# Performance work log

Hardware: AMD Instinct MI355X
Metric: run time of the kernel (lower is better)

The kernel has to match this reference:

```python
import jax, jax.numpy as jnp
import numpy as np

N_NODES = 50000
N_EDGES = 800000
D_IN = 128
D_H = 128
D_OUT = 1
N_GRAPHS = 64
BN_EPS = 1e-5


def _lin(key, i, o):
    return jax.random.normal(key, (i, o), jnp.float32) / np.float32(np.sqrt(i))


def setup_inputs() -> dict:
    key = jax.random.key(0)
    ks = jax.random.split(key, 40)
    inp = {}
    inp["x"] = jax.random.normal(ks[0], (N_NODES, D_IN), jnp.float32)
    inp["edge_index"] = jax.random.randint(ks[1], (2, N_EDGES), 0, N_NODES)
    inp["batch"] = jnp.sort(jax.random.randint(ks[2], (N_NODES,), 0, N_GRAPHS))
    dims = [D_IN, D_H, D_H]
    ki = 3
    for l in range(3):
        inp[f"l{l}_W1"] = _lin(ks[ki], dims[l], D_H); ki += 1
        inp[f"l{l}_b1"] = jnp.zeros((D_H,), jnp.float32)
        inp[f"l{l}_W2"] = _lin(ks[ki], D_H, D_H); ki += 1
        inp[f"l{l}_b2"] = jnp.zeros((D_H,), jnp.float32)
        inp[f"l{l}_g"] = jnp.ones((D_H,), jnp.float32)
        inp[f"l{l}_beta"] = jnp.zeros((D_H,), jnp.float32)
    inp["p_W1"] = _lin(ks[ki], D_H * 3, D_H); ki += 1
    inp["p_b1"] = jnp.zeros((D_H,), jnp.float32)
    inp["p_g"] = jnp.ones((D_H,), jnp.float32)
    inp["p_beta"] = jnp.zeros((D_H,), jnp.float32)
    inp["p_W2"] = _lin(ks[ki], D_H, D_OUT); ki += 1
    inp["p_b2"] = jnp.zeros((D_OUT,), jnp.float32)
    return inp


def _bn(h, g, b):
    # training-mode BatchNorm1d: biased batch statistics over dim 0
    m = h.mean(0)
    v = h.var(0)
    return (h - m) * (g / jnp.sqrt(v + BN_EPS)) + b


def _gin_conv(x, src, dst, W1, b1, W2, b2):
    # scatter-add neighbor aggregation: messages x[src] summed into dst
    agg = jax.ops.segment_sum(x[src], dst, num_segments=N_NODES)
    h = x + agg  # eps = 0 (GINConv default)
    h = jax.nn.relu(h @ W1 + b1)
    return h @ W2 + b2


def reference(x, edge_index, batch,
              l0_W1, l0_b1, l0_W2, l0_b2, l0_g, l0_beta,
              l1_W1, l1_b1, l1_W2, l1_b2, l1_g, l1_beta,
              l2_W1, l2_b1, l2_W2, l2_b2, l2_g, l2_beta,
              p_W1, p_b1, p_g, p_beta, p_W2, p_b2):
    src, dst = edge_index[0], edge_index[1]
    layers = [
        (l0_W1, l0_b1, l0_W2, l0_b2, l0_g, l0_beta),
        (l1_W1, l1_b1, l1_W2, l1_b2, l1_g, l1_beta),
        (l2_W1, l2_b1, l2_W2, l2_b2, l2_g, l2_beta),
    ]
    h = x
    h_list = []
    for (W1, b1, W2, b2, g, beta) in layers:
        h = _gin_conv(h, src, dst, W1, b1, W2, b2)
        h = jax.nn.relu(_bn(h, g, beta))
        # dropout: identity in eval mode
        h_list.append(h)
    # global mean pool per layer, then concat
    cnt = jax.ops.segment_sum(jnp.ones((N_NODES,), jnp.float32), batch,
                              num_segments=N_GRAPHS)
    cnt = jnp.maximum(cnt, 1.0)[:, None]
    pooled = [jax.ops.segment_sum(hh, batch, num_segments=N_GRAPHS) / cnt
              for hh in h_list]
    z = jnp.concatenate(pooled, axis=1)  # [G, 3*D_H]
    # prediction MLP: fc1 -> relu -> bn -> fc2 (dropout identity)
    z = jax.nn.relu(z @ p_W1 + p_b1)
    z = _bn(z, p_g, p_beta)
    return z @ p_W2 + p_b2  # [G, D_OUT]
```

## Files before the change

kernel.cpp:

```cpp
#include <hip/hip_runtime.h>

#define NN 50000
#define NE 800000
#define D  128
#define NG 64
#define BN_EPS 1e-5f
#define SCAN_B 196

typedef __attribute__((ext_vector_type(8))) short short8;
typedef __attribute__((ext_vector_type(4))) float f32x4;

static __device__ inline unsigned short f2bf_rn(float f) {
  unsigned u = __float_as_uint(f);
  unsigned r = (u + 0x7FFF + ((u >> 16) & 1)) >> 16;
  return (unsigned short)r;
}
static __device__ inline float bf2f(unsigned short h) {
  return __uint_as_float((unsigned)h << 16);
}

__global__ void k_hist(const int* __restrict__ dst, int* __restrict__ counts) {
  int e = blockIdx.x * blockDim.x + threadIdx.x;
  if (e < NE) atomicAdd(&counts[dst[e]], 1);
}

__global__ void k_scan1(const int* __restrict__ counts, int* __restrict__ bsum) {
  const int t = threadIdx.x;
  const int i = blockIdx.x * 256 + t;
  int v = (i < NN) ? counts[i] : 0;
  #pragma unroll
  for (int d = 32; d >= 1; d >>= 1) v += __shfl_xor(v, d, 64);
  __shared__ int ws[4];
  if ((t & 63) == 0) ws[t >> 6] = v;
  __syncthreads();
  if (t == 0) bsum[blockIdx.x] = ws[0] + ws[1] + ws[2] + ws[3];
}

__global__ void k_scan2(const int* __restrict__ bsum, int* __restrict__ boff,
                        int* __restrict__ offs) {
  const int t = threadIdx.x, lane = t & 63, w = t >> 6;
  int v = (t < SCAN_B) ? bsum[t] : 0;
  int s = v;
  #pragma unroll
  for (int d = 1; d < 64; d <<= 1) { int u = __shfl_up(s, d, 64); if (lane >= d) s += u; }
  __shared__ int ws[4];
  if (lane == 63) ws[w] = s;
  __syncthreads();
  int add = 0;
  for (int k = 0; k < w; ++k) add += ws[k];
  if (t < SCAN_B) boff[t] = add + s - v;
  if (t == SCAN_B - 1) offs[NN] = add + s;
}

__global__ void k_scan3(const int* __restrict__ counts, const int* __restrict__ boff,
                        int* __restrict__ offs) {
  const int t = threadIdx.x, lane = t & 63, w = t >> 6;
  const int i = blockIdx.x * 256 + t;
  int v = (i < NN) ? counts[i] : 0;
  int s = v;
  #pragma unroll
  for (int d = 1; d < 64; d <<= 1) { int u = __shfl_up(s, d, 64); if (lane >= d) s += u; }
  __shared__ int ws[4];
  if (lane == 63) ws[w] = s;
  __syncthreads();
  int add = 0;
  for (int k = 0; k < w; ++k) add += ws[k];
  if (i < NN) offs[i] = boff[blockIdx.x] + add + s - v;
}

__global__ void k_scatter(const int* __restrict__ src, const int* __restrict__ dst,
                          const int* __restrict__ offs, int* __restrict__ cursor,
                          int* __restrict__ esrc) {
  int e = blockIdx.x * blockDim.x + threadIdx.x;
  if (e < NE) {
    int d = dst[e];
    int p = offs[d] + atomicAdd(&cursor[d], 1);
    esrc[p] = src[e];
  }
}

__global__ void k_gbounds(const int* __restrict__ batch, int* __restrict__ gstart) {
  const int g = threadIdx.x;
  if (g > NG) return;
  int lo = 0, hi = NN;
  while (lo < hi) { int mid = (lo + hi) >> 1; if (batch[mid] < g) lo = mid + 1; else hi = mid; }
  gstart[g] = lo;
}

__global__ __launch_bounds__(256) void k_cvt(const float* __restrict__ X,
                                             unsigned long long* __restrict__ Xb) {
  const int n4 = NN * D / 4;
  for (int i = blockIdx.x * blockDim.x + threadIdx.x; i < n4; i += gridDim.x * blockDim.x) {
    float4 v = ((const float4*)X)[i];
    unsigned long long p = (unsigned long long)f2bf_rn(v.x) |
                           ((unsigned long long)f2bf_rn(v.y) << 16) |
                           ((unsigned long long)f2bf_rn(v.z) << 32) |
                           ((unsigned long long)f2bf_rn(v.w) << 48);
    Xb[i] = p;
  }
}

struct WPtrs { const float* w[6]; };
__global__ void k_prep6(WPtrs ws, short* __restrict__ wb) {
  const int widx = blockIdx.y;
  const float* __restrict__ W = ws.w[widx];
  short* __restrict__ Wh = wb + (size_t)(widx * 2) * 16384;
  short* __restrict__ Wl = Wh + 16384;
  const int idx = blockIdx.x * 256 + threadIdx.x;
  const int k = idx >> 7, c = idx & 127;
  const float v = W[idx];
  const unsigned short h = f2bf_rn(v);
  const unsigned short lo = f2bf_rn(v - bf2f(h));
  const int o = ((k >> 5) * 128 + c) * 32 + (k & 31);
  Wh[o] = (short)h;
  Wl[o] = (short)lo;
}

template<bool BN>
__global__ __launch_bounds__(256) void k_aggregate(const unsigned* __restrict__ Hb,
                                                   const int* __restrict__ offs,
                                                   const int* __restrict__ esrc,
                                                   const float* __restrict__ sums,
                                                   const float* __restrict__ sumsq,
                                                   const float* __restrict__ gw,
                                                   const float* __restrict__ beta,
                                                   float* __restrict__ zstats,
                                                   unsigned* __restrict__ AGGh,
                                                   unsigned* __restrict__ AGGl) {
  if (blockIdx.x == 0 && threadIdx.x < 256) zstats[threadIdx.x] = 0.f;

  const int node = blockIdx.x * 4 + (threadIdx.x >> 6);
  const int lane = threadIdx.x & 63;
  float2 sc = make_float2(1.f, 1.f), sh = make_float2(0.f, 0.f);
  if (BN) {
    const float2 s2 = ((const float2*)sums)[lane];
    const float2 q2 = ((const float2*)sumsq)[lane];
    const float2 g2 = ((const float2*)gw)[lane];
    const float2 b2 = ((const float2*)beta)[lane];
    const float mx = s2.x * (1.f / NN), my = s2.y * (1.f / NN);
    sc.x = g2.x / sqrtf(q2.x * (1.f / NN) - mx * mx + BN_EPS);
    sc.y = g2.y / sqrtf(q2.y * (1.f / NN) - my * my + BN_EPS);
    sh.x = b2.x - mx * sc.x;
    sh.y = b2.y - my * sc.y;
  }

  auto rd = [&](int r) -> float2 {
    const unsigned u = Hb[r * 64 + lane];
    float2 v = make_float2(bf2f((unsigned short)u), bf2f((unsigned short)(u >> 16)));
    if (BN) {
      v.x = fmaxf(fmaf(v.x, sc.x, sh.x), 0.f);
      v.y = fmaxf(fmaf(v.y, sc.y, sh.y), 0.f);
    }
    return v;
  };

  float2 acc = rd(node);
  const int b = offs[node], e = offs[node + 1];
  int i = b;
  for (; i + 8 <= e; i += 8) {
    const int s0 = esrc[i],     s1 = esrc[i + 1], s2 = esrc[i + 2], s3 = esrc[i + 3];
    const int s4 = esrc[i + 4], s5 = esrc[i + 5], s6 = esrc[i + 6], s7 = esrc[i + 7];
    const float2 v0 = rd(s0), v1 = rd(s1), v2 = rd(s2), v3 = rd(s3);
    const float2 v4 = rd(s4), v5 = rd(s5), v6 = rd(s6), v7 = rd(s7);
    acc.x += ((v0.x + v1.x) + (v2.x + v3.x)) + ((v4.x + v5.x) + (v6.x + v7.x));
    acc.y += ((v0.y + v1.y) + (v2.y + v3.y)) + ((v4.y + v5.y) + (v6.y + v7.y));
  }
  for (; i + 4 <= e; i += 4) {
    const int s0 = esrc[i], s1 = esrc[i + 1], s2 = esrc[i + 2], s3 = esrc[i + 3];
    const float2 v0 = rd(s0), v1 = rd(s1), v2 = rd(s2), v3 = rd(s3);
    acc.x += (v0.x + v1.x) + (v2.x + v3.x);
    acc.y += (v0.y + v1.y) + (v2.y + v3.y);
  }
  for (; i < e; ++i) {
    const float2 v = rd(esrc[i]);
    acc.x += v.x; acc.y += v.y;
  }
  const unsigned short hx = f2bf_rn(acc.x), hy = f2bf_rn(acc.y);
  AGGh[node * 64 + lane] = (unsigned)hx | ((unsigned)hy << 16);
  const unsigned short lx = f2bf_rn(acc.x - bf2f(hx)), ly = f2bf_rn(acc.y - bf2f(hy));
  AGGl[node * 64 + lane] = (unsigned)lx | ((unsigned)ly << 16);
}

__global__ __launch_bounds__(512) void k_mlp2(const short* __restrict__ Ah,
                                              const short* __restrict__ Al,
                                              const short* __restrict__ W1h, const short* __restrict__ W1l,
                                              const short* __restrict__ W2h, const short* __restrict__ W2l,
                                              const float* __restrict__ b1, const float* __restrict__ b2,
                                              short* __restrict__ Hb,
                                              float* __restrict__ stats) {
  __shared__ __align__(16) short regA[32768];
  __shared__ __align__(16) short regB[32768];

  const int t = threadIdx.x;
  {
    const short8* __restrict__ g1h = (const short8*)W1h;
    const short8* __restrict__ g1l = (const short8*)W1l;
    const short8* __restrict__ g2h = (const short8*)W2h;
    const short8* __restrict__ g2l = (const short8*)W2l;
    short8* a8 = (short8*)regA;
    short8* b8 = (short8*)regB;
    #pragma unroll
    for (int i = 0; i < 4; ++i) {
      a8[i * 512 + t]        = g1h[i * 512 + t];
      a8[2048 + i * 512 + t] = g1l[i * 512 + t];
      b8[i * 512 + t]        = g2h[i * 512 + t];
      b8[2048 + i * 512 + t] = g2l[i * 512 + t];
    }
  }

  const int l = t & 63, w = t >> 6;
  const int lr = l & 15, fq = l >> 4, lk = fq * 8;
  const int tile0 = blockIdx.x * 128 + w * 16;
  const int arow = tile0 + lr;
  const bool rowok = arow < NN;

  short8 ah[4], al[4];
  {
    const short8 z = (short8)(0);
    #pragma unroll
    for (int kc = 0; kc < 4; ++kc) {
      ah[kc] = rowok ? *(const short8*)(Ah + (size_t)arow * D + kc * 32 + lk) : z;
      al[kc] = rowok ? *(const short8*)(Al + (size_t)arow * D + kc * 32 + lk) : z;
    }
  }
  __syncthreads();

  f32x4 acc[8];
  #pragma unroll
  for (int ct = 0; ct < 8; ++ct) acc[ct] = (f32x4)(0.f);
  #pragma unroll
  for (int kc = 0; kc < 4; ++kc) {
    #pragma unroll
    for (int ct = 0; ct < 8; ++ct) {
      const short8 bh = *(const short8*)(&regA[(kc * 128 + ct * 16 + lr) * 32 + lk]);
      const short8 bl = *(const short8*)(&regA[16384 + (kc * 128 + ct * 16 + lr) * 32 + lk]);
      acc[ct] = __builtin_amdgcn_mfma_f32_16x16x32_bf16(ah[kc], bh, acc[ct], 0, 0, 0);
      acc[ct] = __builtin_amdgcn_mfma_f32_16x16x32_bf16(al[kc], bh, acc[ct], 0, 0, 0);
      acc[ct] = __builtin_amdgcn_mfma_f32_16x16x32_bf16(ah[kc], bl, acc[ct], 0, 0, 0);
    }
  }
  __syncthreads();

  #pragma unroll
  for (int ct = 0; ct < 8; ++ct) {
    const float bb = b1[ct * 16 + lr];
    #pragma unroll
    for (int j = 0; j < 4; ++j) {
      const int r = w * 16 + fq * 4 + j;
      const int swc = (ct * 16 + lr) ^ ((r & 7) << 3);
      const float v = fmaxf(acc[ct][j] + bb, 0.f);
      const unsigned short h = f2bf_rn(v);
      regA[r * 128 + swc] = (short)h;
      regA[16384 + r * 128 + swc] = (short)f2bf_rn(v - bf2f(h));
    }
  }
  __syncthreads();

  f32x4 acc2[8];
  #pragma unroll
  for (int ct = 0; ct < 8; ++ct) acc2[ct] = (f32x4)(0.f);
  {
    const int r = w * 16 + lr;
    const int sx = (r & 7) << 3;
    short8 ch[4], cl[4];
    #pragma unroll
    for (int kc = 0; kc < 4; ++kc) {
      const int swb = r * 128 + ((kc * 32 + lk) ^ sx);
      ch[kc] = *(const short8*)(regA + swb);
      cl[kc] = *(const short8*)(regA + 16384 + swb);
    }
    #pragma unroll
    for (int kc = 0; kc < 4; ++kc) {
      #pragma unroll
      for (int ct = 0; ct < 8; ++ct) {
        const short8 bh = *(const short8*)(&regB[(kc * 128 + ct * 16 + lr) * 32 + lk]);
        const short8 bl = *(const short8*)(&regB[16384 + (kc * 128 + ct * 16 + lr) * 32 + lk]);
        acc2[ct] = __builtin_amdgcn_mfma_f32_16x16x32_bf16(ch[kc], bh, acc2[ct], 0, 0, 0);
        acc2[ct] = __builtin_amdgcn_mfma_f32_16x16x32_bf16(cl[kc], bh, acc2[ct], 0, 0, 0);
        acc2[ct] = __builtin_amdgcn_mfma_f32_16x16x32_bf16(ch[kc], bl, acc2[ct], 0, 0, 0);
      }
    }
  }

  float ps[8], pq[8];
  #pragma unroll
  for (int ct = 0; ct < 8; ++ct) { ps[ct] = 0.f; pq[ct] = 0.f; }
  #pragma unroll
  for (int ct = 0; ct < 8; ++ct) {
    const float bb = b2[ct * 16 + lr];
    #pragma unroll
    for (int j = 0; j < 4; ++j) {
      const int gr = tile0 + fq * 4 + j;
      if (gr < NN) {
        const float v = acc2[ct][j] + bb;
        Hb[(size_t)gr * D + ct * 16 + lr] = (short)f2bf_rn(v);
        ps[ct] += v; pq[ct] += v * v;
      }
    }
  }
  __syncthreads();
  float* red  = (float*)regA;
  float* redq = red + 4096;
  const int grp = w * 4 + fq;
  #pragma unroll
  for (int ct = 0; ct < 8; ++ct) {
    red [grp * 128 + ct * 16 + lr] = ps[ct];
    redq[grp * 128 + ct * 16 + lr] = pq[ct];
  }
  __syncthreads();
  if (t < 128) {
    float s = 0.f, q = 0.f;
    #pragma unroll
    for (int g2 = 0; g2 < 32; ++g2) { s += red[g2 * 128 + t]; q += redq[g2 * 128 + t]; }
    atomicAdd(&stats[t], s);
    atomicAdd(&stats[128 + t], q);
  }
}

__global__ __launch_bounds__(256) void k_pool(const unsigned short* __restrict__ Hb,
                                              const float* __restrict__ sums,
                                              const float* __restrict__ sumsq,
                                              const float* __restrict__ gw,
                                              const float* __restrict__ beta,
                                              const int* __restrict__ gstart,
                                              float* __restrict__ pooled, int lofs) {
  const int g = blockIdx.y;
  const int s = gstart[g], e = gstart[g + 1];
  const int t = threadIdx.x, c = t & 127, half = t >> 7;
  const float m  = sums[c] * (1.f / NN);
  const float sc = gw[c] / sqrtf(sumsq[c] * (1.f / NN) - m * m + BN_EPS);
  const float sh = beta[c] - m * sc;
  const int len = e - s;
  const int nchunk = (int)gridDim.x;
  const int per = (len + nchunk - 1) / nchunk;
  const int r0 = s + (int)blockIdx.x * per;
  const int r1 = min(e, r0 + per);
  float sum = 0.f;
  for (int r = r0 + half; r < r1; r += 2)
    sum += fmaxf(fmaf(bf2f(Hb[r * D + c]), sc, sh), 0.f);
  __shared__ float red[256];
  red[t] = sum;
  __syncthreads();
  if (t < 128) atomicAdd(&pooled[g * 384 + lofs + c], red[t] + red[t + 128]);
}

__global__ __launch_bounds__(128) void k_fc1(const float* __restrict__ pooled,
                                             const int* __restrict__ gstart,
                                             const float* __restrict__ W1,
                                             const float* __restrict__ b1,
                                             float* __restrict__ z1) {
  const int g = blockIdx.x, j = threadIdx.x;
  __shared__ float p[384];
  const float cnt = (float)(gstart[g + 1] - gstart[g]);
  const float inv = 1.f / fmaxf(cnt, 1.f);
  for (int k = j; k < 384; k += 128) p[k] = pooled[g * 384 + k] * inv;
  __syncthreads();
  float acc = b1[j];
  #pragma unroll 8
  for (int k = 0; k < 384; ++k) acc = fmaf(p[k], W1[k * 128 + j], acc);
  z1[g * 128 + j] = fmaxf(acc, 0.f);
}

__global__ __launch_bounds__(128) void k_head(const float* __restrict__ z1,
                                              const float* __restrict__ g,
                                              const float* __restrict__ beta,
                                              const float* __restrict__ W2,
                                              const float* __restrict__ b2,
                                              float* __restrict__ out) {
  __shared__ float z2[NG][129];
  __shared__ float w2s[128];
  const int j = threadIdx.x;
  w2s[j] = W2[j];
  float vals[NG];
  float s = 0.f, q = 0.f;
  for (int gg = 0; gg < NG; ++gg) {
    float v = z1[gg * 128 + j];
    vals[gg] = v; s += v; q += v * v;
  }
  const float m   = s / (float)NG;
  const float var = q / (float)NG - m * m;
  const float sc  = g[j] / sqrtf(var + BN_EPS);
  const float sh  = beta[j] - m * sc;
  for (int gg = 0; gg < NG; ++gg) z2[gg][j] = vals[gg] * sc + sh;
  __syncthreads();
  if (j < NG) {
    float acc = b2[0];
    #pragma unroll 8
    for (int k = 0; k < 128; ++k) acc += z2[j][k] * w2s[k];
    out[j] = acc;
  }
}

extern "C" void kernel_launch(void* const* d_in, const int* in_sizes, int n_in,
                              void* d_out, int out_size, void* d_ws, size_t ws_size,
                              hipStream_t stream) {
  const float* x     = (const float*)d_in[0];
  const int*   e_src = (const int*)d_in[1];
  const int*   e_dst = e_src + NE;
  const int*   batch = (const int*)d_in[2];
  const float *lW1[3], *lb1[3], *lW2[3], *lb2[3], *lg[3], *lbeta[3];
  for (int l = 0; l < 3; ++l) {
    lW1[l]   = (const float*)d_in[3 + 6 * l + 0];
    lb1[l]   = (const float*)d_in[3 + 6 * l + 1];
    lW2[l]   = (const float*)d_in[3 + 6 * l + 2];
    lb2[l]   = (const float*)d_in[3 + 6 * l + 3];
    lg[l]    = (const float*)d_in[3 + 6 * l + 4];
    lbeta[l] = (const float*)d_in[3 + 6 * l + 5];
  }
  const float* pW1   = (const float*)d_in[21];
  const float* pb1   = (const float*)d_in[22];
  const float* pg    = (const float*)d_in[23];
  const float* pbeta = (const float*)d_in[24];
  const float* pW2   = (const float*)d_in[25];
  const float* pb2   = (const float*)d_in[26];
  float* out = (float*)d_out;

  char* w = (char*)d_ws;
  auto alloc = [&](size_t bytes) { char* p = w; w += (bytes + 255) & ~(size_t)255; return p; };
  short* AGGh   = (short*)alloc((size_t)NN * D * 2);
  short* AGGl   = (short*)alloc((size_t)NN * D * 2);
  short* Hb0    = (short*)alloc((size_t)NN * D * 2);
  short* Hb1    = (short*)alloc((size_t)NN * D * 2);
  short* xb     = Hb1;
  int*   counts = (int*)alloc((size_t)NN * 4);
  int*   cursor = (int*)alloc((size_t)NN * 4);
  int*   offs   = (int*)alloc((size_t)(NN + 1) * 4);
  int*   esrc   = (int*)alloc((size_t)NE * 4);
  int*   bsum   = (int*)alloc((size_t)SCAN_B * 4);
  int*   boff   = (int*)alloc((size_t)SCAN_B * 4);
  int*   gstart = (int*)alloc((size_t)(NG + 1) * 4);
  float* stats  = (float*)alloc((size_t)3 * 256 * 4);
  float* pooled = (float*)alloc((size_t)NG * 384 * 4);
  float* z1     = (float*)alloc((size_t)NG * 128 * 4);
  short* wb     = (short*)alloc((size_t)12 * 32768);
  auto st = [&](int l) { return stats + (size_t)l * 256; };

  hipMemsetAsync(counts, 0, (size_t)NN * 4, stream);
  hipMemsetAsync(cursor, 0, (size_t)NN * 4, stream);
  hipMemsetAsync(pooled, 0, (size_t)NG * 384 * 4, stream);

  k_hist   <<<(NE + 255) / 256, 256, 0, stream>>>(e_dst, counts);
  k_scan1  <<<SCAN_B, 256, 0, stream>>>(counts, bsum);
  k_scan2  <<<1, 256, 0, stream>>>(bsum, boff, offs);
  k_scan3  <<<SCAN_B, 256, 0, stream>>>(counts, boff, offs);
  k_scatter<<<(NE + 255) / 256, 256, 0, stream>>>(e_src, e_dst, offs, cursor, esrc);
  k_gbounds<<<1, 128, 0, stream>>>(batch, gstart);
  k_cvt    <<<1024, 256, 0, stream>>>(x, (unsigned long long*)xb);

  WPtrs ws;
  ws.w[0] = lW1[0]; ws.w[1] = lW2[0];
  ws.w[2] = lW1[1]; ws.w[3] = lW2[1];
  ws.w[4] = lW1[2]; ws.w[5] = lW2[2];
  k_prep6<<<dim3(64, 6), 256, 0, stream>>>(ws, wb);
  auto plane = [&](int widx, int hilo) { return wb + (size_t)(widx * 2 + hilo) * 16384; };

  short* Hbuf[2] = {Hb0, Hb1};
  const int mlp_grid = (NN + 127) / 128;
  for (int l = 0; l < 3; ++l) {
    if (l == 0)
      k_aggregate<false><<<NN / 4, 256, 0, stream>>>((const unsigned*)xb, offs, esrc,
                                                     nullptr, nullptr, nullptr, nullptr,
                                                     st(0), (unsigned*)AGGh, (unsigned*)AGGl);
    else
      k_aggregate<true><<<NN / 4, 256, 0, stream>>>((const unsigned*)Hbuf[(l - 1) & 1], offs, esrc,
                                                    st(l - 1), st(l - 1) + 128, lg[l - 1], lbeta[l - 1],
                                                    st(l), (unsigned*)AGGh, (unsigned*)AGGl);
    k_mlp2<<<mlp_grid, 512, 0, stream>>>(AGGh, AGGl,
                                         plane(2 * l, 0), plane(2 * l, 1),
                                         plane(2 * l + 1, 0), plane(2 * l + 1, 1),
                                         lb1[l], lb2[l], Hbuf[l & 1], st(l));
    k_pool <<<dim3(8, NG), 256, 0, stream>>>((const unsigned short*)Hbuf[l & 1],
                                             st(l), st(l) + 128, lg[l], lbeta[l],
                                             gstart, pooled, l * 128);
  }

  k_fc1 <<<NG, 128, 0, stream>>>(pooled, gstart, pW1, pb1, z1);
  k_head<<<1, 128, 0, stream>>>(z1, pg, pbeta, pW2, pb2, out);
}
```

Measured before the change: 390.7 us.

## Retile fused MLP warps into 2x4 row/column tiles for LDS weight reuse

Each of the 8 wavefronts now computes a 32-row by 64-column tile (two row tiles, four column tiles) instead of 16 rows by all 128 columns. Every weight fragment read from LDS is reused across two row tiles, halving the B-operand LDS reads per MFMA in both GEMMs. The stats reduction buffer shrinks to 16 groups with padded stride 132 to limit bank conflicts. The trade-off is that each wave loads twice as many A-row fragments and holds more registers for them.

```diff
diff --git a/kernel.cpp b/kernel.cpp
--- a/kernel.cpp
+++ b/kernel.cpp
@@ -210,108 +210,131 @@
 
   const int l = t & 63, w = t >> 6;
   const int lr = l & 15, fq = l >> 4, lk = fq * 8;
-  const int tile0 = blockIdx.x * 128 + w * 16;
-  const int arow = tile0 + lr;
-  const bool rowok = arow < NN;
-
-  short8 ah[4], al[4];
+  const int rg = w & 3;
+  const int cg = w >> 2;
+  const int row0 = blockIdx.x * 128;
+
+  short8 ah[2][4], al[2][4];
   {
     const short8 z = (short8)(0);
     #pragma unroll
-    for (int kc = 0; kc < 4; ++kc) {
-      ah[kc] = rowok ? *(const short8*)(Ah + (size_t)arow * D + kc * 32 + lk) : z;
-      al[kc] = rowok ? *(const short8*)(Al + (size_t)arow * D + kc * 32 + lk) : z;
-    }
-  }
-  __syncthreads();
-
-  f32x4 acc[8];
-  #pragma unroll
-  for (int ct = 0; ct < 8; ++ct) acc[ct] = (f32x4)(0.f);
+    for (int rt = 0; rt < 2; ++rt) {
+      const int arow = row0 + rg * 32 + rt * 16 + lr;
+      const bool ok = arow < NN;
+      #pragma unroll
+      for (int kc = 0; kc < 4; ++kc) {
+        ah[rt][kc] = ok ? *(const short8*)(Ah + (size_t)arow * D + kc * 32 + lk) : z;
+        al[rt][kc] = ok ? *(const short8*)(Al + (size_t)arow * D + kc * 32 + lk) : z;
+      }
+    }
+  }
+  __syncthreads();
+
+  f32x4 acc[2][4];
+  #pragma unroll
+  for (int rt = 0; rt < 2; ++rt)
+    #pragma unroll
+    for (int ct = 0; ct < 4; ++ct) acc[rt][ct] = (f32x4)(0.f);
   #pragma unroll
   for (int kc = 0; kc < 4; ++kc) {
     #pragma unroll
-    for (int ct = 0; ct < 8; ++ct) {
-      const short8 bh = *(const short8*)(&regA[(kc * 128 + ct * 16 + lr) * 32 + lk]);
-      const short8 bl = *(const short8*)(&regA[16384 + (kc * 128 + ct * 16 + lr) * 32 + lk]);
-      acc[ct] = __builtin_amdgcn_mfma_f32_16x16x32_bf16(ah[kc], bh, acc[ct], 0, 0, 0);
-      acc[ct] = __builtin_amdgcn_mfma_f32_16x16x32_bf16(al[kc], bh, acc[ct], 0, 0, 0);
-      acc[ct] = __builtin_amdgcn_mfma_f32_16x16x32_bf16(ah[kc], bl, acc[ct], 0, 0, 0);
-    }
-  }
-  __syncthreads();
-
-  #pragma unroll
-  for (int ct = 0; ct < 8; ++ct) {
-    const float bb = b1[ct * 16 + lr];
-    #pragma unroll
-    for (int j = 0; j < 4; ++j) {
-      const int r = w * 16 + fq * 4 + j;
-      const int swc = (ct * 16 + lr) ^ ((r & 7) << 3);
-      const float v = fmaxf(acc[ct][j] + bb, 0.f);
-      const unsigned short h = f2bf_rn(v);
-      regA[r * 128 + swc] = (short)h;
-      regA[16384 + r * 128 + swc] = (short)f2bf_rn(v - bf2f(h));
-    }
-  }
-  __syncthreads();
-
-  f32x4 acc2[8];
-  #pragma unroll
-  for (int ct = 0; ct < 8; ++ct) acc2[ct] = (f32x4)(0.f);
-  {
-    const int r = w * 16 + lr;
-    const int sx = (r & 7) << 3;
-    short8 ch[4], cl[4];
-    #pragma unroll
-    for (int kc = 0; kc < 4; ++kc) {
-      const int swb = r * 128 + ((kc * 32 + lk) ^ sx);
-      ch[kc] = *(const short8*)(regA + swb);
-      cl[kc] = *(const short8*)(regA + 16384 + swb);
-    }
-    #pragma unroll
-    for (int kc = 0; kc < 4; ++kc) {
+    for (int ct = 0; ct < 4; ++ct) {
+      const int wc = cg * 64 + ct * 16 + lr;
+      const short8 bh = *(const short8*)(&regA[(kc * 128 + wc) * 32 + lk]);
+      const short8 bl = *(const short8*)(&regA[16384 + (kc * 128 + wc) * 32 + lk]);
       #pragma unroll
-      for (int ct = 0; ct < 8; ++ct) {
-        const short8 bh = *(const short8*)(&regB[(kc * 128 + ct * 16 + lr) * 32 + lk]);
-        const short8 bl = *(const short8*)(&regB[16384 + (kc * 128 + ct * 16 + lr) * 32 + lk]);
-        acc2[ct] = __builtin_amdgcn_mfma_f32_16x16x32_bf16(ch[kc], bh, acc2[ct], 0, 0, 0);
-        acc2[ct] = __builtin_amdgcn_mfma_f32_16x16x32_bf16(cl[kc], bh, acc2[ct], 0, 0, 0);
-        acc2[ct] = __builtin_amdgcn_mfma_f32_16x16x32_bf16(ch[kc], bl, acc2[ct], 0, 0, 0);
+      for (int rt = 0; rt < 2; ++rt) {
+        acc[rt][ct] = __builtin_amdgcn_mfma_f32_16x16x32_bf16(ah[rt][kc], bh, acc[rt][ct], 0, 0, 0);
+        acc[rt][ct] = __builtin_amdgcn_mfma_f32_16x16x32_bf16(al[rt][kc], bh, acc[rt][ct], 0, 0, 0);
+        acc[rt][ct] = __builtin_amdgcn_mfma_f32_16x16x32_bf16(ah[rt][kc], bl, acc[rt][ct], 0, 0, 0);
       }
     }
   }
-
-  float ps[8], pq[8];
-  #pragma unroll
-  for (int ct = 0; ct < 8; ++ct) { ps[ct] = 0.f; pq[ct] = 0.f; }
-  #pragma unroll
-  for (int ct = 0; ct < 8; ++ct) {
-    const float bb = b2[ct * 16 + lr];
-    #pragma unroll
-    for (int j = 0; j < 4; ++j) {
-      const int gr = tile0 + fq * 4 + j;
-      if (gr < NN) {
-        const float v = acc2[ct][j] + bb;
-        Hb[(size_t)gr * D + ct * 16 + lr] = (short)f2bf_rn(v);
-        ps[ct] += v; pq[ct] += v * v;
+  __syncthreads();
+
+  #pragma unroll
+  for (int rt = 0; rt < 2; ++rt) {
+    #pragma unroll
+    for (int ct = 0; ct < 4; ++ct) {
+      const int c = cg * 64 + ct * 16 + lr;
+      const float bb = b1[c];
+      #pragma unroll
+      for (int j = 0; j < 4; ++j) {
+        const int r = rg * 32 + rt * 16 + fq * 4 + j;
+        const int swc = c ^ ((r & 7) << 3);
+        const float v = fmaxf(acc[rt][ct][j] + bb, 0.f);
+        const unsigned short h = f2bf_rn(v);
+        regA[r * 128 + swc] = (short)h;
+        regA[16384 + r * 128 + swc] = (short)f2bf_rn(v - bf2f(h));
       }
     }
   }
   __syncthreads();
+
+  f32x4 acc2[2][4];
+  #pragma unroll
+  for (int rt = 0; rt < 2; ++rt)
+    #pragma unroll
+    for (int ct = 0; ct < 4; ++ct) acc2[rt][ct] = (f32x4)(0.f);
+  #pragma unroll
+  for (int kc = 0; kc < 4; ++kc) {
+    short8 ch[2], cl[2];
+    #pragma unroll
+    for (int rt = 0; rt < 2; ++rt) {
+      const int r = rg * 32 + rt * 16 + lr;
+      const int swb = r * 128 + ((kc * 32 + lk) ^ ((r & 7) << 3));
+      ch[rt] = *(const short8*)(regA + swb);
+      cl[rt] = *(const short8*)(regA + 16384 + swb);
+    }
+    #pragma unroll
+    for (int ct = 0; ct < 4; ++ct) {
+      const int wc = cg * 64 + ct * 16 + lr;
+      const short8 bh = *(const short8*)(&regB[(kc * 128 + wc) * 32 + lk]);
+      const short8 bl = *(const short8*)(&regB[16384 + (kc * 128 + wc) * 32 + lk]);
+      #pragma unroll
+      for (int rt = 0; rt < 2; ++rt) {
+        acc2[rt][ct] = __builtin_amdgcn_mfma_f32_16x16x32_bf16(ch[rt], bh, acc2[rt][ct], 0, 0, 0);
+        acc2[rt][ct] = __builtin_amdgcn_mfma_f32_16x16x32_bf16(cl[rt], bh, acc2[rt][ct], 0, 0, 0);
+        acc2[rt][ct] = __builtin_amdgcn_mfma_f32_16x16x32_bf16(ch[rt], bl, acc2[rt][ct], 0, 0, 0);
+      }
+    }
+  }
+
+  float ps[4], pq[4];
+  #pragma unroll
+  for (int ct = 0; ct < 4; ++ct) { ps[ct] = 0.f; pq[ct] = 0.f; }
+  #pragma unroll
+  for (int rt = 0; rt < 2; ++rt) {
+    #pragma unroll
+    for (int ct = 0; ct < 4; ++ct) {
+      const int c = cg * 64 + ct * 16 + lr;
+      const float bb = b2[c];
+      #pragma unroll
+      for (int j = 0; j < 4; ++j) {
+        const int gr = row0 + rg * 32 + rt * 16 + fq * 4 + j;
+        if (gr < NN) {
+          const float v = acc2[rt][ct][j] + bb;
+          Hb[(size_t)gr * D + c] = (short)f2bf_rn(v);
+          ps[ct] += v; pq[ct] += v * v;
+        }
+      }
+    }
+  }
+  __syncthreads();
   float* red  = (float*)regA;
-  float* redq = red + 4096;
-  const int grp = w * 4 + fq;
-  #pragma unroll
-  for (int ct = 0; ct < 8; ++ct) {
-    red [grp * 128 + ct * 16 + lr] = ps[ct];
-    redq[grp * 128 + ct * 16 + lr] = pq[ct];
+  float* redq = red + 16 * 132;
+  const int grp = rg * 4 + fq;
+  #pragma unroll
+  for (int ct = 0; ct < 4; ++ct) {
+    const int c = cg * 64 + ct * 16 + lr;
+    red [grp * 132 + c] = ps[ct];
+    redq[grp * 132 + c] = pq[ct];
   }
   __syncthreads();
   if (t < 128) {
     float s = 0.f, q = 0.f;
     #pragma unroll
-    for (int g2 = 0; g2 < 32; ++g2) { s += red[g2 * 128 + t]; q += redq[g2 * 128 + t]; }
+    for (int g2 = 0; g2 < 16; ++g2) { s += red[g2 * 132 + t]; q += redq[g2 * 132 + t]; }
     atomicAdd(&stats[t], s);
     atomicAdd(&stats[128 + t], q);
   }
```

New measurement: 389.0 us. Within noise of the previous version (-0.4%).
